# Kernel optimization log

Hardware: AMD Instinct MI355X
Metric: run time of the kernel (lower is better)

The kernel has to match this reference:

```python
import jax, jax.numpy as jnp
import numpy as np

N, C, H, W = 16, 256, 64, 64
KC, VC, HEADS = 256, 256, 8

def setup_inputs() -> dict:
    key = jax.random.key(0)
    ks = jax.random.split(key, 9)
    s = 0.02
    return {
        "x": jax.random.normal(ks[0], (N, C, H, W), dtype=jnp.float32),
        "Wk": jax.random.normal(ks[1], (KC, C), dtype=jnp.float32) * s,
        "bk": jax.random.normal(ks[2], (KC,), dtype=jnp.float32) * s,
        "Wq": jax.random.normal(ks[3], (KC, C), dtype=jnp.float32) * s,
        "bq": jax.random.normal(ks[4], (KC,), dtype=jnp.float32) * s,
        "Wv": jax.random.normal(ks[5], (VC, C), dtype=jnp.float32) * s,
        "bv": jax.random.normal(ks[6], (VC,), dtype=jnp.float32) * s,
        "Wr": jax.random.normal(ks[7], (C, VC), dtype=jnp.float32) * s,
        "br": jax.random.normal(ks[8], (C,), dtype=jnp.float32) * s,
    }

def reference(x, Wk, bk, Wq, bq, Wv, bv, Wr, br):
    n, c, h, w = x.shape
    hw = h * w
    hk = KC // HEADS   # per-head key channels
    hv = VC // HEADS   # per-head value channels
    # 1x1 convs as channel matmuls
    keys = jnp.einsum('oi,nihw->nohw', Wk, x) + bk[None, :, None, None]
    queries = jnp.einsum('oi,nihw->nohw', Wq, x) + bq[None, :, None, None]
    values = jnp.einsum('oi,nihw->nohw', Wv, x) + bv[None, :, None, None]
    # split heads: (n, heads, ch_per_head, hw)
    k = keys.reshape(n, HEADS, hk, hw)
    q = queries.reshape(n, HEADS, hk, hw)
    v = values.reshape(n, HEADS, hv, hw)
    k = jax.nn.softmax(k, axis=3)   # softmax over spatial positions
    q = jax.nn.softmax(q, axis=2)   # softmax over key channels
    # context: (n, heads, hk, hv)
    ctx = jnp.einsum('nhkl,nhvl->nhkv', k, v)
    # attended: (n, heads, hv, hw)
    att = jnp.einsum('nhkv,nhkl->nhvl', ctx, q)
    agg = att.reshape(n, VC, h, w)
    out = jnp.einsum('ov,nvhw->nohw', Wr, agg) + br[None, :, None, None] + x
    return out
```

## Files before the change

kernel.cpp:

```cpp
#include <hip/hip_runtime.h>

#define NB   16
#define CD   256
#define HWD  4096

typedef __attribute__((ext_vector_type(8))) short short8;
typedef __attribute__((ext_vector_type(4))) float f32x4;

static __device__ __forceinline__ float b2f(unsigned short u) {
  union { unsigned int i; float f; } x; x.i = ((unsigned int)u) << 16; return x.f;
}
static __device__ __forceinline__ unsigned short f2b(float f) {
  union { float f; unsigned int i; } x; x.f = f;
  return (unsigned short)((x.i + 0x7fffu + ((x.i >> 16) & 1u)) >> 16);
}

static __device__ __forceinline__ void gload16(const void* g, const unsigned short* l) {
  __builtin_amdgcn_global_load_lds(
      (const __attribute__((address_space(1))) void*)g,
      (__attribute__((address_space(3))) void*)l, 16, 0, 0);
}

__global__ __launch_bounds__(256)
void prep_kernel(const float* __restrict__ Wk, const float* __restrict__ Wq,
                 const float* __restrict__ Wv, unsigned short* __restrict__ Wc)
{
  int e4 = blockIdx.x * 256 + threadIdx.x;
  int base = e4 * 4;
  int w = base >> 16, off = base & 65535;
  const float* W = (w == 0) ? Wk : (w == 1) ? Wq : Wv;
  f32x4 v = *(const f32x4*)(W + off);
  unsigned int lo = (unsigned int)f2b(v.x) | ((unsigned int)f2b(v.y) << 16);
  unsigned int hi = (unsigned int)f2b(v.z) | ((unsigned int)f2b(v.w) << 16);
  *(uint2*)(Wc + base) = make_uint2(lo, hi);
}

__global__ __launch_bounds__(256)
void xt_kernel(const float* __restrict__ x, unsigned short* __restrict__ xT)
{
  __shared__ __align__(16) unsigned short T[64 * 80];
  const int t = threadIdx.x;
  const int l0 = blockIdx.x * 64, c0 = blockIdx.y * 64, n = blockIdx.z;
  const float* xn = x + (size_t)n * CD * HWD;
#pragma unroll
  for (int i = 0; i < 4; ++i) {
    int idx = t + i * 256;
    int c = idx >> 4, l4 = (idx & 15) * 4;
    f32x4 v = *(const f32x4*)(xn + (size_t)(c0 + c) * HWD + l0 + l4);
    T[(l4 + 0) * 80 + c] = f2b(v.x);
    T[(l4 + 1) * 80 + c] = f2b(v.y);
    T[(l4 + 2) * 80 + c] = f2b(v.z);
    T[(l4 + 3) * 80 + c] = f2b(v.w);
  }
  __syncthreads();
  unsigned short* dst = xT + ((size_t)n * HWD + l0) * CD + c0;
#pragma unroll
  for (int i = 0; i < 2; ++i) {
    int e = t + i * 256;
    int lr = e >> 3, c8 = (e & 7) * 8;
    *(short8*)(dst + (size_t)lr * CD + c8) = *(const short8*)(T + lr * 80 + c8);
  }
}

__global__ __launch_bounds__(256, 4)
void kqv_kernel(const unsigned short* __restrict__ Wc,
                const unsigned short* __restrict__ xT,
                const float* __restrict__ bk, const float* __restrict__ bq,
                const float* __restrict__ bv,
                unsigned short* __restrict__ ekeys,
                unsigned short* __restrict__ qsmT,
                unsigned short* __restrict__ vals)
{
  __shared__ __align__(16) unsigned short smem[17408];

  const int t  = threadIdx.x;
  const int lt = blockIdx.x;
  const int mt = blockIdx.y;
  const int n  = blockIdx.z;
  const int l0 = lt * 128;
  const int m0 = mt * 128;
  const int wsel = m0 >> 8;
  const int ocbase = m0 & 255;

  const unsigned short* Ag  = Wc;
  const unsigned short* Btn = xT + (size_t)n * HWD * CD;

  const int w = t >> 6, lane = t & 63;
  const int wr = (w >> 1) * 64, wc = (w & 1) * 64;
  const int lhi = lane >> 4, llo = lane & 15;

  f32x4 acc[4][4] = {};

  auto stage = [&](int buf, int ks) {
    unsigned short* As = smem + buf * 8192;
    unsigned short* Bs = As + 4096;
    const int k0 = ks * 32;
#pragma unroll
    for (int i = 0; i < 2; ++i) {
      int s   = t + i * 256;
      int row = s >> 2;
      int src = (((s ^ row) & 3)) << 3;
      gload16(Ag  + (size_t)(m0 + row) * CD + k0 + src, As + s * 8);
      gload16(Btn + (size_t)(l0 + row) * CD + k0 + src, Bs + s * 8);
    }
  };

  stage(0, 0);
  stage(1, 1);
#pragma unroll
  for (int ks = 0; ks < 8; ++ks) {
    if (ks < 7) asm volatile("s_waitcnt vmcnt(4)" ::: "memory");
    else        asm volatile("s_waitcnt vmcnt(0)" ::: "memory");
    asm volatile("s_barrier" ::: "memory");

    const unsigned short* As = smem + (ks & 1) * 8192;
    const unsigned short* Bs = As + 4096;
    const int slot = (lhi ^ (llo & 3)) * 8;
    short8 a[4], b[4];
#pragma unroll
    for (int mi = 0; mi < 4; ++mi)
      a[mi] = *(const short8*)(As + (wr + mi * 16 + llo) * 32 + slot);
#pragma unroll
    for (int ni = 0; ni < 4; ++ni)
      b[ni] = *(const short8*)(Bs + (wc + ni * 16 + llo) * 32 + slot);

    asm volatile("s_waitcnt lgkmcnt(0)" ::: "memory");
    asm volatile("s_barrier" ::: "memory");

    if (ks < 6) stage(ks & 1, ks + 2);

#pragma unroll
    for (int mi = 0; mi < 4; ++mi)
#pragma unroll
      for (int ni = 0; ni < 4; ++ni)
        acc[mi][ni] = __builtin_amdgcn_mfma_f32_16x16x32_bf16(a[mi], b[ni], acc[mi][ni], 0, 0, 0);
  }

  const float* bias = (wsel == 0) ? bk : (wsel == 1) ? bq : bv;

  if (wsel == 1) {
#pragma unroll
    for (int mi = 0; mi < 4; ++mi)
#pragma unroll
      for (int r = 0; r < 4; ++r) {
        float bb = bias[ocbase + wr + mi * 16 + lhi * 4 + r];
#pragma unroll
        for (int ni = 0; ni < 4; ++ni) acc[mi][ni][r] += bb;
      }
#pragma unroll
    for (int g = 0; g < 2; ++g) {
#pragma unroll
      for (int ni = 0; ni < 4; ++ni) {
        float m = -1e30f;
#pragma unroll
        for (int mi = 2 * g; mi < 2 * g + 2; ++mi)
#pragma unroll
          for (int r = 0; r < 4; ++r) m = fmaxf(m, acc[mi][ni][r]);
        m = fmaxf(m, __shfl_xor(m, 16));
        m = fmaxf(m, __shfl_xor(m, 32));
        float s = 0.f;
#pragma unroll
        for (int mi = 2 * g; mi < 2 * g + 2; ++mi)
#pragma unroll
          for (int r = 0; r < 4; ++r) {
            float e = __expf(acc[mi][ni][r] - m);
            acc[mi][ni][r] = e;
            s += e;
          }
        s += __shfl_xor(s, 16);
        s += __shfl_xor(s, 32);
        float inv = 1.f / s;
#pragma unroll
        for (int mi = 2 * g; mi < 2 * g + 2; ++mi)
#pragma unroll
          for (int r = 0; r < 4; ++r) acc[mi][ni][r] *= inv;
      }
    }
    unsigned short* Co2 = smem;
#pragma unroll
    for (int mi = 0; mi < 4; ++mi)
#pragma unroll
      for (int ni = 0; ni < 4; ++ni) {
        int col = wc + ni * 16 + llo;
#pragma unroll
        for (int r = 0; r < 4; ++r) {
          int row = wr + mi * 16 + lhi * 4 + r;
          Co2[col * 136 + row] = f2b(acc[mi][ni][r]);
        }
      }
    __syncthreads();
    unsigned short* dst = qsmT + ((size_t)n * HWD + l0) * CD + ocbase;
#pragma unroll
    for (int i = 0; i < 8; ++i) {
      int e = t + i * 256;
      int l = e >> 4, c8 = (e & 15) * 8;
      *(short8*)(dst + (size_t)l * CD + c8) = *(const short8*)(Co2 + l * 136 + c8);
    }
  } else {
    unsigned short* Co = smem;
#pragma unroll
    for (int mi = 0; mi < 4; ++mi)
#pragma unroll
      for (int ni = 0; ni < 4; ++ni) {
        int col = wc + ni * 16 + llo;
#pragma unroll
        for (int r = 0; r < 4; ++r) {
          int row = wr + mi * 16 + lhi * 4 + r;
          float val = acc[mi][ni][r] + bias[ocbase + row];
          if (wsel == 0) val = __expf(val);
          Co[row * 136 + col] = f2b(val);
        }
      }
    __syncthreads();
    unsigned short* dst = ((wsel == 0) ? ekeys : vals)
                          + ((size_t)(n * CD + ocbase)) * HWD + l0;
#pragma unroll
    for (int i = 0; i < 8; ++i) {
      int e = t + i * 256;
      int row = e >> 4, c8 = (e & 15) * 8;
      *(short8*)(dst + (size_t)row * HWD + c8) = *(const short8*)(Co + row * 136 + c8);
    }
  }
}

__global__ __launch_bounds__(256)
void rowsum_kernel(const unsigned short* __restrict__ ekeys,
                   float* __restrict__ stats)
{
  __shared__ float red[4];
  const int r = blockIdx.x;
  const int t = threadIdx.x;
  const unsigned short* rowp = ekeys + (size_t)r * HWD;
  float s = 0.f;
#pragma unroll
  for (int i = 0; i < 2; ++i) {
    const short8 u = *(const short8*)(rowp + t * 8 + i * 2048);
#pragma unroll
    for (int j = 0; j < 8; ++j) s += b2f((unsigned short)u[j]);
  }
#pragma unroll
  for (int off = 1; off < 64; off <<= 1) s += __shfl_xor(s, off);
  if ((t & 63) == 0) red[t >> 6] = s;
  __syncthreads();
  if (t == 0) stats[r] = 1.f / (red[0] + red[1] + red[2] + red[3]);
}

__global__ __launch_bounds__(256)
void ctx_kernel(const unsigned short* __restrict__ ekeys,
                const unsigned short* __restrict__ vals,
                const float* __restrict__ stats,
                float* __restrict__ ctxp)
{
  __shared__ float Cs[4][32][33];
  const int hf = blockIdx.x;
  const int nh = blockIdx.y;
  const int n = nh >> 3, h = nh & 7;
  const int t = threadIdx.x, w = t >> 6, lane = t & 63;
  const int lhi = lane >> 4, llo = lane & 15;
  const int lbase = hf * 2048 + w * 512;

  const unsigned short* kr = ekeys + (size_t)(n * CD + h * 32) * HWD;
  const unsigned short* vr = vals + (size_t)(n * CD + h * 32) * HWD;

  float inv[2];
#pragma unroll
  for (int mi = 0; mi < 2; ++mi)
    inv[mi] = stats[n * CD + h * 32 + mi * 16 + llo];

  f32x4 acc[2][2] = {};
  for (int ks = 0; ks < 16; ++ks) {
    const int loff = lbase + ks * 32 + lhi * 8;
    short8 a[2], b[2];
#pragma unroll
    for (int mi = 0; mi < 2; ++mi) {
      const short8 u = *(const short8*)(kr + (size_t)(mi * 16 + llo) * HWD + loff);
      short8 af;
#pragma unroll
      for (int j = 0; j < 8; ++j)
        af[j] = (short)f2b(b2f((unsigned short)u[j]) * inv[mi]);
      a[mi] = af;
    }
#pragma unroll
    for (int ni = 0; ni < 2; ++ni)
      b[ni] = *(const short8*)(vr + (size_t)(ni * 16 + llo) * HWD + loff);
    acc[0][0] = __builtin_amdgcn_mfma_f32_16x16x32_bf16(a[0], b[0], acc[0][0], 0, 0, 0);
    acc[0][1] = __builtin_amdgcn_mfma_f32_16x16x32_bf16(a[0], b[1], acc[0][1], 0, 0, 0);
    acc[1][0] = __builtin_amdgcn_mfma_f32_16x16x32_bf16(a[1], b[0], acc[1][0], 0, 0, 0);
    acc[1][1] = __builtin_amdgcn_mfma_f32_16x16x32_bf16(a[1], b[1], acc[1][1], 0, 0, 0);
  }

#pragma unroll
  for (int mi = 0; mi < 2; ++mi)
#pragma unroll
    for (int ni = 0; ni < 2; ++ni)
#pragma unroll
      for (int r = 0; r < 4; ++r)
        Cs[w][mi * 16 + lhi * 4 + r][ni * 16 + llo] = acc[mi][ni][r];
  __syncthreads();
#pragma unroll
  for (int i = 0; i < 4; ++i) {
    int e = t + i * 256;
    int kc = e >> 5, vc = e & 31;
    float sum = Cs[0][kc][vc] + Cs[1][kc][vc] + Cs[2][kc][vc] + Cs[3][kc][vc];
    ctxp[((size_t)hf * 128 + nh) * 1024 + e] = sum;
  }
}

__global__ __launch_bounds__(256)
void proj_kernel(const float* __restrict__ ctxp, const float* __restrict__ Wr,
                 unsigned short* __restrict__ M)
{
  __shared__ float cs[32][33];
  const int nh = blockIdx.x;
  const int n = nh >> 3, h = nh & 7;
  const int t = threadIdx.x;
#pragma unroll
  for (int i = 0; i < 4; ++i) {
    int e = t + i * 256;
    cs[e >> 5][e & 31] = ctxp[(size_t)nh * 1024 + e] + ctxp[((size_t)128 + nh) * 1024 + e];
  }
  __syncthreads();
  float wreg[32];
  const float* wp = Wr + (size_t)t * 256 + h * 32;
#pragma unroll
  for (int i = 0; i < 8; ++i) {
    f32x4 v = *(const f32x4*)(wp + i * 4);
    wreg[i * 4] = v.x; wreg[i * 4 + 1] = v.y; wreg[i * 4 + 2] = v.z; wreg[i * 4 + 3] = v.w;
  }
  unsigned short o16[32];
#pragma unroll
  for (int kc = 0; kc < 32; ++kc) {
    float s = 0.f;
#pragma unroll
    for (int vv = 0; vv < 32; ++vv) s += wreg[vv] * cs[kc][vv];
    o16[kc] = f2b(s);
  }
  unsigned short* mp = M + (size_t)(n * CD + t) * 256 + h * 32;
#pragma unroll
  for (int i = 0; i < 8; ++i) {
    unsigned int lo = (unsigned int)o16[i * 4]     | ((unsigned int)o16[i * 4 + 1] << 16);
    unsigned int hi = (unsigned int)o16[i * 4 + 2] | ((unsigned int)o16[i * 4 + 3] << 16);
    *(uint2*)(mp + i * 4) = make_uint2(lo, hi);
  }
}

__global__ __launch_bounds__(256, 2)
void out_kernel(const unsigned short* __restrict__ M,
                const unsigned short* __restrict__ qsmT,
                const float* __restrict__ br,
                const float* __restrict__ x,
                float* __restrict__ out)
{
  __shared__ __align__(16) unsigned short smem[32768];
  unsigned short* As = smem;
  unsigned short* Bs = smem + 16384;

  const int t  = threadIdx.x;
  const int lt = blockIdx.x;
  const int mt = blockIdx.y;
  const int n  = blockIdx.z;
  const int l0 = lt * 64, m0 = mt * 64;

  const unsigned short* Ag  = M + (size_t)n * CD * 256;
  const unsigned short* Btn = qsmT + (size_t)n * HWD * CD;

  const int wid = t >> 6, lane = t & 63;
  const int wr = (wid >> 1) * 32, wc = (wid & 1) * 32;
  const int lhi = lane >> 4, llo = lane & 15;

#pragma unroll
  for (int i = 0; i < 8; ++i) {
    int s = t + i * 256;
    int R = s >> 5, sl = s & 31;
    int srcsl = (sl & 24) | ((sl ^ R) & 7);
    gload16(Ag  + (size_t)(m0 + R) * CD + srcsl * 8, As + s * 8);
    gload16(Btn + (size_t)(l0 + R) * CD + srcsl * 8, Bs + s * 8);
  }
  __syncthreads();

  f32x4 acc[2][2] = {};
#pragma unroll
  for (int ks = 0; ks < 8; ++ks) {
    int jg = ks * 4 + lhi;
    short8 a[2], b[2];
#pragma unroll
    for (int mi = 0; mi < 2; ++mi) {
      int R = wr + mi * 16 + llo;
      int pj = (jg & 24) | ((jg ^ (R & 7)) & 7);
      a[mi] = *(const short8*)(As + R * 256 + pj * 8);
    }
#pragma unroll
    for (int ni = 0; ni < 2; ++ni) {
      int l = wc + ni * 16 + llo;
      int pj = (jg & 24) | ((jg ^ (l & 7)) & 7);
      b[ni] = *(const short8*)(Bs + l * 256 + pj * 8);
    }
#pragma unroll
    for (int mi = 0; mi < 2; ++mi)
#pragma unroll
      for (int ni = 0; ni < 2; ++ni)
        acc[mi][ni] = __builtin_amdgcn_mfma_f32_16x16x32_bf16(a[mi], b[ni], acc[mi][ni], 0, 0, 0);
  }

  const float* xn = x + (size_t)n * CD * HWD;
  float* on = out + (size_t)n * CD * HWD;
#pragma unroll
  for (int mi = 0; mi < 2; ++mi)
#pragma unroll
    for (int r = 0; r < 4; ++r) {
      int row = m0 + wr + mi * 16 + lhi * 4 + r;
      float bb = br[row];
#pragma unroll
      for (int ni = 0; ni < 2; ++ni) {
        int col = l0 + wc + ni * 16 + llo;
        size_t off = (size_t)row * HWD + col;
        on[off] = acc[mi][ni][r] + bb + xn[off];
      }
    }
}

extern "C" void kernel_launch(void* const* d_in, const int* in_sizes, int n_in,
                              void* d_out, int out_size, void* d_ws, size_t ws_size,
                              hipStream_t stream) {
  const float* x  = (const float*)d_in[0];
  const float* Wk = (const float*)d_in[1];
  const float* bk = (const float*)d_in[2];
  const float* Wq = (const float*)d_in[3];
  const float* bq = (const float*)d_in[4];
  const float* Wv = (const float*)d_in[5];
  const float* bv = (const float*)d_in[6];
  const float* Wr = (const float*)d_in[7];
  const float* br = (const float*)d_in[8];
  float* out = (float*)d_out;

  char* ws = (char*)d_ws;
  unsigned short* ekeys = (unsigned short*)(ws);
  unsigned short* vals  = (unsigned short*)(ws + 33554432);
  unsigned short* qsmT  = (unsigned short*)(ws + 67108864);
  float* stats          = (float*)(ws + 100663296);
  float* ctxp           = (float*)(ws + 100696064);
  unsigned short* M     = (unsigned short*)(ws + 101744640);
  unsigned short* Wc    = (unsigned short*)(ws + 103841792);
  unsigned short* xT    = (unsigned short*)d_out;

  hipLaunchKernelGGL(prep_kernel, dim3(192), dim3(256), 0, stream, Wk, Wq, Wv, Wc);
  hipLaunchKernelGGL(xt_kernel, dim3(64, 4, NB), dim3(256), 0, stream, x, xT);
  hipLaunchKernelGGL(kqv_kernel, dim3(32, 6, NB), dim3(256), 0, stream,
                     Wc, xT, bk, bq, bv, ekeys, qsmT, vals);
  hipLaunchKernelGGL(rowsum_kernel, dim3(NB * CD), dim3(256), 0, stream, ekeys, stats);
  hipLaunchKernelGGL(ctx_kernel, dim3(2, 128), dim3(256), 0, stream,
                     ekeys, vals, stats, ctxp);
  hipLaunchKernelGGL(proj_kernel, dim3(128), dim3(256), 0, stream, ctxp, Wr, M);
  hipLaunchKernelGGL(out_kernel, dim3(64, 4, NB), dim3(256), 0, stream,
                     M, qsmT, br, x, out);
}
```

Baseline: 130.1 us.

## Enlarge out_kernel tiles with double-buffered K pipeline and split ctx reduction wider

out_kernel moves from 64x64 tiles that load the full K=256 panel at once to 128x128 tiles. It streams K in 32-wide chunks through a double-buffered, swizzled LDS pipeline with explicit vmcnt waits and barriers, and each wave computes a 4x4 grid of MFMA tiles. This raises data reuse per byte loaded, overlaps global loads with MFMA work, and halves LDS use so occupancy can rise. ctx_kernel now splits the spatial reduction 8 ways instead of 2 for more blocks, proj_kernel sums 8 partials, and the partial buffer moves into unused space in the output. The cost is higher register pressure and more hand-written synchronization in the out kernel.

```diff
diff --git a/kernel.cpp b/kernel.cpp
--- a/kernel.cpp
+++ b/kernel.cpp
@@ -257,7 +257,7 @@
   const int n = nh >> 3, h = nh & 7;
   const int t = threadIdx.x, w = t >> 6, lane = t & 63;
   const int lhi = lane >> 4, llo = lane & 15;
-  const int lbase = hf * 2048 + w * 512;
+  const int lbase = hf * 512 + w * 128;
 
   const unsigned short* kr = ekeys + (size_t)(n * CD + h * 32) * HWD;
   const unsigned short* vr = vals + (size_t)(n * CD + h * 32) * HWD;
@@ -268,7 +268,8 @@
     inv[mi] = stats[n * CD + h * 32 + mi * 16 + llo];
 
   f32x4 acc[2][2] = {};
-  for (int ks = 0; ks < 16; ++ks) {
+#pragma unroll
+  for (int ks = 0; ks < 4; ++ks) {
     const int loff = lbase + ks * 32 + lhi * 8;
     short8 a[2], b[2];
 #pragma unroll
@@ -317,7 +318,11 @@
 #pragma unroll
   for (int i = 0; i < 4; ++i) {
     int e = t + i * 256;
-    cs[e >> 5][e & 31] = ctxp[(size_t)nh * 1024 + e] + ctxp[((size_t)128 + nh) * 1024 + e];
+    float s = 0.f;
+#pragma unroll
+    for (int p = 0; p < 8; ++p)
+      s += ctxp[((size_t)p * 128 + nh) * 1024 + e];
+    cs[e >> 5][e & 31] = s;
   }
   __syncthreads();
   float wreg[32];
@@ -344,74 +349,85 @@
   }
 }
 
-__global__ __launch_bounds__(256, 2)
+__global__ __launch_bounds__(256, 4)
 void out_kernel(const unsigned short* __restrict__ M,
                 const unsigned short* __restrict__ qsmT,
                 const float* __restrict__ br,
                 const float* __restrict__ x,
                 float* __restrict__ out)
 {
-  __shared__ __align__(16) unsigned short smem[32768];
-  unsigned short* As = smem;
-  unsigned short* Bs = smem + 16384;
+  __shared__ __align__(16) unsigned short smem[16384];
 
   const int t  = threadIdx.x;
   const int lt = blockIdx.x;
   const int mt = blockIdx.y;
   const int n  = blockIdx.z;
-  const int l0 = lt * 64, m0 = mt * 64;
+  const int l0 = lt * 128, m0 = mt * 128;
 
   const unsigned short* Ag  = M + (size_t)n * CD * 256;
   const unsigned short* Btn = qsmT + (size_t)n * HWD * CD;
 
-  const int wid = t >> 6, lane = t & 63;
-  const int wr = (wid >> 1) * 32, wc = (wid & 1) * 32;
+  const int w = t >> 6, lane = t & 63;
+  const int wr = (w >> 1) * 64, wc = (w & 1) * 64;
   const int lhi = lane >> 4, llo = lane & 15;
 
-#pragma unroll
-  for (int i = 0; i < 8; ++i) {
-    int s = t + i * 256;
-    int R = s >> 5, sl = s & 31;
-    int srcsl = (sl & 24) | ((sl ^ R) & 7);
-    gload16(Ag  + (size_t)(m0 + R) * CD + srcsl * 8, As + s * 8);
-    gload16(Btn + (size_t)(l0 + R) * CD + srcsl * 8, Bs + s * 8);
-  }
-  __syncthreads();
-
-  f32x4 acc[2][2] = {};
+  f32x4 acc[4][4] = {};
+
+  auto stage = [&](int buf, int ks) {
+    unsigned short* As = smem + buf * 8192;
+    unsigned short* Bs = As + 4096;
+    const int k0 = ks * 32;
+#pragma unroll
+    for (int i = 0; i < 2; ++i) {
+      int s   = t + i * 256;
+      int row = s >> 2;
+      int src = (((s ^ row) & 3)) << 3;
+      gload16(Ag  + (size_t)(m0 + row) * CD + k0 + src, As + s * 8);
+      gload16(Btn + (size_t)(l0 + row) * CD + k0 + src, Bs + s * 8);
+    }
+  };
+
+  stage(0, 0);
+  stage(1, 1);
 #pragma unroll
   for (int ks = 0; ks < 8; ++ks) {
-    int jg = ks * 4 + lhi;
-    short8 a[2], b[2];
-#pragma unroll
-    for (int mi = 0; mi < 2; ++mi) {
-      int R = wr + mi * 16 + llo;
-      int pj = (jg & 24) | ((jg ^ (R & 7)) & 7);
-      a[mi] = *(const short8*)(As + R * 256 + pj * 8);
-    }
-#pragma unroll
-    for (int ni = 0; ni < 2; ++ni) {
-      int l = wc + ni * 16 + llo;
-      int pj = (jg & 24) | ((jg ^ (l & 7)) & 7);
-      b[ni] = *(const short8*)(Bs + l * 256 + pj * 8);
-    }
-#pragma unroll
-    for (int mi = 0; mi < 2; ++mi)
-#pragma unroll
-      for (int ni = 0; ni < 2; ++ni)
+    if (ks < 7) asm volatile("s_waitcnt vmcnt(4)" ::: "memory");
+    else        asm volatile("s_waitcnt vmcnt(0)" ::: "memory");
+    asm volatile("s_barrier" ::: "memory");
+
+    const unsigned short* As = smem + (ks & 1) * 8192;
+    const unsigned short* Bs = As + 4096;
+    const int slot = (lhi ^ (llo & 3)) * 8;
+    short8 a[4], b[4];
+#pragma unroll
+    for (int mi = 0; mi < 4; ++mi)
+      a[mi] = *(const short8*)(As + (wr + mi * 16 + llo) * 32 + slot);
+#pragma unroll
+    for (int ni = 0; ni < 4; ++ni)
+      b[ni] = *(const short8*)(Bs + (wc + ni * 16 + llo) * 32 + slot);
+
+    asm volatile("s_waitcnt lgkmcnt(0)" ::: "memory");
+    asm volatile("s_barrier" ::: "memory");
+
+    if (ks < 6) stage(ks & 1, ks + 2);
+
+#pragma unroll
+    for (int mi = 0; mi < 4; ++mi)
+#pragma unroll
+      for (int ni = 0; ni < 4; ++ni)
         acc[mi][ni] = __builtin_amdgcn_mfma_f32_16x16x32_bf16(a[mi], b[ni], acc[mi][ni], 0, 0, 0);
   }
 
   const float* xn = x + (size_t)n * CD * HWD;
   float* on = out + (size_t)n * CD * HWD;
 #pragma unroll
-  for (int mi = 0; mi < 2; ++mi)
+  for (int mi = 0; mi < 4; ++mi)
 #pragma unroll
     for (int r = 0; r < 4; ++r) {
       int row = m0 + wr + mi * 16 + lhi * 4 + r;
       float bb = br[row];
 #pragma unroll
-      for (int ni = 0; ni < 2; ++ni) {
+      for (int ni = 0; ni < 4; ++ni) {
         int col = l0 + wc + ni * 16 + llo;
         size_t off = (size_t)row * HWD + col;
         on[off] = acc[mi][ni][r] + bb + xn[off];
@@ -438,19 +454,19 @@
   unsigned short* vals  = (unsigned short*)(ws + 33554432);
   unsigned short* qsmT  = (unsigned short*)(ws + 67108864);
   float* stats          = (float*)(ws + 100663296);
-  float* ctxp           = (float*)(ws + 100696064);
   unsigned short* M     = (unsigned short*)(ws + 101744640);
   unsigned short* Wc    = (unsigned short*)(ws + 103841792);
   unsigned short* xT    = (unsigned short*)d_out;
+  float* ctxp           = (float*)((char*)d_out + 33554432);
 
   hipLaunchKernelGGL(prep_kernel, dim3(192), dim3(256), 0, stream, Wk, Wq, Wv, Wc);
   hipLaunchKernelGGL(xt_kernel, dim3(64, 4, NB), dim3(256), 0, stream, x, xT);
   hipLaunchKernelGGL(kqv_kernel, dim3(32, 6, NB), dim3(256), 0, stream,
                      Wc, xT, bk, bq, bv, ekeys, qsmT, vals);
   hipLaunchKernelGGL(rowsum_kernel, dim3(NB * CD), dim3(256), 0, stream, ekeys, stats);
-  hipLaunchKernelGGL(ctx_kernel, dim3(2, 128), dim3(256), 0, stream,
+  hipLaunchKernelGGL(ctx_kernel, dim3(8, 128), dim3(256), 0, stream,
                      ekeys, vals, stats, ctxp);
   hipLaunchKernelGGL(proj_kernel, dim3(128), dim3(256), 0, stream, ctxp, Wr, M);
-  hipLaunchKernelGGL(out_kernel, dim3(64, 4, NB), dim3(256), 0, stream,
+  hipLaunchKernelGGL(out_kernel, dim3(32, 2, NB), dim3(256), 0, stream,
                      M, qsmT, br, x, out);
 }
```

Measured after the change: 131.7 us. No clear change (+1.2%).
